# Kernel tuning notes

Measured on AMD Instinct MI355X. Metric: run time of the kernel, lower is better.

## Reference

```python
import jax, jax.numpy as jnp
import numpy as np
from jax import lax


def _causal_mask(shape, mask_center):
    # shape = (out_ch, in_ch, h, w); mirrors CausalConv2d mask construction
    o, i, h, w = shape
    m = np.zeros(shape, dtype=np.float32)
    m[:, :, : h // 2, :] = 1.0
    m[:, :, h // 2, : w // 2 + (0 if mask_center else 1)] = 1.0
    return jnp.asarray(m)

MASK1 = _causal_mask((16, 1, 7, 7), mask_center=True)
MASK2 = _causal_mask((16, 16, 3, 3), mask_center=False)


def _conv(x, w, b, pad):
    y = lax.conv_general_dilated(
        x, w, window_strides=(1, 1), padding=[(pad, pad), (pad, pad)],
        dimension_numbers=("NCHW", "OIHW", "NCHW"))
    return y + b[None, :, None, None]


def setup_inputs() -> dict:
    key = jax.random.key(0)
    ks = jax.random.split(key, 7)
    B, H, W = 1024, 64, 64
    x = jax.random.uniform(ks[0], (B, 1, H, W), dtype=jnp.float32)
    # Kaiming-ish init scales
    w1 = jax.random.normal(ks[1], (16, 1, 7, 7), jnp.float32) * (1.0 / np.sqrt(1 * 49))
    b1 = jax.random.normal(ks[2], (16,), jnp.float32) * 0.01
    w2 = jax.random.normal(ks[3], (16, 16, 3, 3), jnp.float32) * (1.0 / np.sqrt(16 * 9))
    b2 = jax.random.normal(ks[4], (16,), jnp.float32) * 0.01
    w3 = jax.random.normal(ks[5], (1, 16, 1, 1), jnp.float32) * (1.0 / np.sqrt(16))
    b3 = jax.random.normal(ks[6], (1,), jnp.float32) * 0.01
    return {"x": x, "w1": w1, "b1": b1, "w2": w2, "b2": b2, "w3": w3, "b3": b3}


def reference(x, w1, b1, w2, b2, w3, b3):
    # PixelCNN._forward: masked conv7x7 -> relu -> masked conv3x3 -> relu -> conv1x1 -> sigmoid
    h = jax.nn.relu(_conv(x, w1 * MASK1, b1, pad=3))
    h = jax.nn.relu(_conv(h, w2 * MASK2, b2, pad=1))
    return jax.nn.sigmoid(_conv(h, w3, b3, pad=0))
```

## Files before the change

kernel.cpp:

```cpp
#include <hip/hip_runtime.h>

typedef _Float16 half8  __attribute__((ext_vector_type(8)));
typedef __fp16   fp16x2 __attribute__((ext_vector_type(2)));
typedef float    floatx4 __attribute__((ext_vector_type(4)));

#define IMG_H 64
#define IMG_W 64
#define TH 16
#define TW 32
#define INW 40
#define H1W 34
#define NPX 640
#define CP 912
#define CPM1 911

__device__ __forceinline__ unsigned pk2u(float a, float b) {
    fp16x2 h = __builtin_amdgcn_cvt_pkrtz(a, b);
    return __builtin_bit_cast(unsigned, h);
}

__global__ __launch_bounds__(256, 8) void pixelcnn_mfma10(
    const float* __restrict__ x,
    const float* __restrict__ w1, const float* __restrict__ b1,
    const float* __restrict__ w2, const float* __restrict__ b2,
    const float* __restrict__ w3, const float* __restrict__ b3,
    float* __restrict__ out)
{
    __shared__ __align__(16) _Float16      s16[4 * CP];
    __shared__ __align__(16) _Float16      s_w1t[16 * 32];
    __shared__ __align__(16) unsigned char s_w2t8[16 * 96];
    __shared__ __align__(16) float         s_b1[16], s_b2[16], s_w3[16];
    __shared__ float                       s_b3;
    __shared__ __align__(16) unsigned      s_h1[2 * NPX * 2];

    const int t    = threadIdx.x;
    const int lane = t & 63;
    const int wave = t >> 6;
    const int n    = lane & 15;
    const int quad = lane >> 4;
    const int img  = blockIdx.y;
    const int btile = blockIdx.x;
    const int ty0 = (btile >> 1) * TH;
    const int tx0 = (btile & 1) * TW;

    const float* xim = x + img * (IMG_H * IMG_W);

    if (t < 210) {
        int r = t / 10, c4 = (t - r * 10) * 4;
        int gy = ty0 - 4 + r;
        int gx0 = tx0 - 4 + c4;
        float4 v  = {0.f, 0.f, 0.f, 0.f};
        float4 v2 = {0.f, 0.f, 0.f, 0.f};
        if ((unsigned)gy < IMG_H) {
            const float* rp = xim + gy * IMG_W;
            if ((unsigned)gx0 < IMG_W)       v  = *(const float4*)(rp + gx0);
            if ((unsigned)(gx0 + 4) < IMG_W) v2 = *(const float4*)(rp + gx0 + 4);
        }
        unsigned a0 = pk2u(v.x,  v.y),  a1 = pk2u(v.z,  v.w);
        unsigned a2 = pk2u(v2.x, v2.y), a3 = pk2u(v2.z, v2.w);
        unsigned m10 = (a0 >> 16) | (a1 << 16);
        unsigned m21 = (a1 >> 16) | (a2 << 16);
        unsigned m32 = (a2 >> 16) | (a3 << 16);
        int lin = r * INW + c4;
        *(uint2*)&s16[0*CP + 4 + lin + 0] = uint2{a0,  a1 };
        *(uint2*)&s16[1*CP + 3 + lin + 1] = uint2{m10, m21};
        *(uint2*)&s16[2*CP + 2 + lin + 2] = uint2{a1,  a2 };
        *(uint2*)&s16[3*CP + 1 + lin + 3] = uint2{m21, m32};
    }
    if (t < 192) {
        int c = t / 48, e = t - c * 48;
        s16[c * CP + (4 - c) + 840 + e] = (_Float16)0.f;
    }
    {
        int ch = t >> 4, l = t & 15;
        const float* w1c = w1 + ch * 49;
#pragma unroll
        for (int j2 = 0; j2 < 2; ++j2) {
            int k = l + 16 * j2, q = k >> 3, jj = k & 7;
            float v = 0.f;
            if (q < 3)      { if (jj < 7) v = w1c[q * 7 + jj]; }
            else            { if (jj < 3) v = w1c[21 + jj];    }
            s_w1t[ch * 32 + k] = (_Float16)v;
        }
        const float* w2cl = w2 + (ch * 16 + l) * 9;
#pragma unroll
        for (int j = 0; j < 6; ++j) {
            float v = (j < 5) ? w2cl[j] : 0.f;
            unsigned q8 = (unsigned)__builtin_amdgcn_cvt_pk_fp8_f32(v, 0.f, 0, false);
            s_w2t8[ch * 96 + j * 16 + l] = (unsigned char)(q8 & 0xff);
        }
    }
    if (t < 16) { s_b1[t] = b1[t]; s_b2[t] = b2[t]; s_w3[t] = w3[t]; }
    if (t == 16) s_b3 = b3[0];
    __syncthreads();

    {
        const half8 afrag = *(const half8*)&s_w1t[n * 32 + quad * 8];
        const floatx4 bias1 = ((const floatx4*)s_b1)[quad];
        int p  = wave * 16 + n;
        int py = (p >= H1W) ? 1 : 0;
        int px = p - py * H1W;
        int lin1p = (py + quad) * INW + px + 4;
        unsigned wd = (unsigned)((quad >> 1) * (NPX * 2) + p * 2 + (quad & 1));

#pragma unroll
        for (int i = 0; i < 10; ++i) {
            int c = px & 3;
            const _Float16* ap = &s16[c * CPM1 + lin1p];
            uint2 lo = *(const uint2*)ap;
            uint2 hi = *(const uint2*)(ap + 4);
            uint4 bu; bu.x = lo.x; bu.y = lo.y; bu.z = hi.x; bu.w = hi.y;
            half8 b = __builtin_bit_cast(half8, bu);
            floatx4 acc = bias1;
            acc = __builtin_amdgcn_mfma_f32_16x16x32_f16(afrag, b, acc, 0, 0, 0);
            int d = __builtin_amdgcn_cvt_pk_fp8_f32(fmaxf(acc[0], 0.f), fmaxf(acc[1], 0.f), 0, false);
            d = __builtin_amdgcn_cvt_pk_fp8_f32(fmaxf(acc[2], 0.f), fmaxf(acc[3], 0.f), d, true);
            s_h1[wd] = (unsigned)d;
            int px2 = px + 30;
            bool wrap = px2 >= H1W;
            px     = wrap ? px2 - H1W : px2;
            lin1p += wrap ? 76 : 70;
            wd    += 128;
        }
    }
    __syncthreads();

    {
        int cell = -1;
        if (t < 34)      { if (ty0 == 0) cell = t; }
        else if (t < 52) { cell = (t - 34) * H1W + ((tx0 == 0) ? 0 : 33); }
        if (cell >= 0) {
            *(uint2*)&s_h1[cell * 2]           = uint2{0u, 0u};
            *(uint2*)&s_h1[NPX * 2 + cell * 2] = uint2{0u, 0u};
        }
    }
    __syncthreads();

    {
        const long w2f0 = *(const long*)&s_w2t8[n * 96 +  0 + quad * 8];
        const long w2f1 = *(const long*)&s_w2t8[n * 96 + 32 + quad * 8];
        const long w2f2 = *(const long*)&s_w2t8[n * 96 + 64 + quad * 8];
        const floatx4 bias2 = ((const floatx4*)s_b2)[quad];
        const floatx4 w3q   = ((const floatx4*)s_w3)[quad];
        const float bias3 = s_b3;
        const int y0 = wave >> 1, x0 = (wave & 1) * 16;
        const int tqh = quad >> 1, plane = quad & 1;
        const int E0 = (y0 + 1) * H1W + x0 + n + 1;
        const char* h1b = (const char*)s_h1 + plane * (NPX * 8);
        const char* a0 = h1b + (E0 - 35 + tqh) * 8;
        const char* a1 = h1b + (E0 + (tqh ? -1 : -33)) * 8;
        const char* a2 = h1b + E0 * 8;
        float* sbase = out + ((img * IMG_H) + ty0 + y0 + 2 * quad) * IMG_W + tx0 + x0 + n;

#pragma unroll
        for (int g = 0; g < 2; ++g) {
            float sv0, sv1, sv2, sv3;
#pragma unroll
            for (int q = 0; q < 4; ++q) {
                const int k = g * 4 + q;
                floatx4 acc = bias2;
                acc = __builtin_amdgcn_mfma_f32_16x16x32_fp8_fp8(w2f0, *(const long*)(a0 + k * 544), acc, 0, 0, 0);
                acc = __builtin_amdgcn_mfma_f32_16x16x32_fp8_fp8(w2f1, *(const long*)(a1 + k * 544), acc, 0, 0, 0);
                acc = __builtin_amdgcn_mfma_f32_16x16x32_fp8_fp8(w2f2, *(const long*)(a2 + k * 544), acc, 0, 0, 0);
                float s = fmaxf(acc[0], 0.f) * w3q[0];
                s = fmaf(fmaxf(acc[1], 0.f), w3q[1], s);
                s = fmaf(fmaxf(acc[2], 0.f), w3q[2], s);
                s = fmaf(fmaxf(acc[3], 0.f), w3q[3], s);
                s += __shfl_xor(s, 16);
                s += __shfl_xor(s, 32);
                if      (q == 0) sv0 = s;
                else if (q == 1) sv1 = s;
                else if (q == 2) sv2 = s;
                else             sv3 = s;
            }
            float t01 = (quad & 1) ? sv1 : sv0;
            float t23 = (quad & 1) ? sv3 : sv2;
            float v   = (quad & 2) ? t23 : t01;
            float r = __builtin_amdgcn_rcpf(1.f + __expf(-(v + bias3)));
            *(float*)((char*)sbase + g * 2048) = r;
        }
    }
}

extern "C" void kernel_launch(void* const* d_in, const int* in_sizes, int n_in,
                              void* d_out, int out_size, void* d_ws, size_t ws_size,
                              hipStream_t stream) {
    const float* x  = (const float*)d_in[0];
    const float* w1 = (const float*)d_in[1];
    const float* b1 = (const float*)d_in[2];
    const float* w2 = (const float*)d_in[3];
    const float* b2 = (const float*)d_in[4];
    const float* w3 = (const float*)d_in[5];
    const float* b3 = (const float*)d_in[6];
    float* out = (float*)d_out;

    dim3 grid(8, 1024);
    dim3 block(256);
    hipLaunchKernelGGL(pixelcnn_mfma10, grid, block, 0, stream,
                       x, w1, b1, w2, b2, w3, b3, out);
}
```

Before: 108.5 us.

## Retile to full-width 8-row strips, removing column halos and a barrier

Each block now covers an 8x64 strip of the image instead of a 16x32 tile, so no left or right column halo is needed. The conv1 stage processes 9 rows of 66 columns with simpler, fixed addressing and no per-iteration wrap logic. Zeroing of the padding borders moves into the load phase and is handled by predication in the conv1 store, which removes one __syncthreads. The cost is a larger top/bottom halo relative to tile size, about 9/8 conv1 recompute instead of 10/8, with different LDS layout strides.

```diff
diff --git a/kernel.cpp b/kernel.cpp
--- a/kernel.cpp
+++ b/kernel.cpp
@@ -6,11 +6,12 @@
 
 #define IMG_H 64
 #define IMG_W 64
-#define TH 16
-#define TW 32
-#define INW 40
-#define H1W 34
-#define NPX 640
+#define TH 8
+#define INW 72
+#define INH 12
+#define H1W 66
+#define H1H 9
+#define PLDW (H1H*H1W*2)
 #define CP 912
 #define CPM1 911
 
@@ -19,7 +20,7 @@
     return __builtin_bit_cast(unsigned, h);
 }
 
-__global__ __launch_bounds__(256, 8) void pixelcnn_mfma10(
+__global__ __launch_bounds__(256, 8) void pixelcnn_mfma11(
     const float* __restrict__ x,
     const float* __restrict__ w1, const float* __restrict__ b1,
     const float* __restrict__ w2, const float* __restrict__ b2,
@@ -31,7 +32,7 @@
     __shared__ __align__(16) unsigned char s_w2t8[16 * 96];
     __shared__ __align__(16) float         s_b1[16], s_b2[16], s_w3[16];
     __shared__ float                       s_b3;
-    __shared__ __align__(16) unsigned      s_h1[2 * NPX * 2];
+    __shared__ __align__(16) unsigned      s_h1[2 * PLDW];
 
     const int t    = threadIdx.x;
     const int lane = t & 63;
@@ -39,16 +40,14 @@
     const int n    = lane & 15;
     const int quad = lane >> 4;
     const int img  = blockIdx.y;
-    const int btile = blockIdx.x;
-    const int ty0 = (btile >> 1) * TH;
-    const int tx0 = (btile & 1) * TW;
+    const int ty0  = blockIdx.x * TH;
 
     const float* xim = x + img * (IMG_H * IMG_W);
 
-    if (t < 210) {
-        int r = t / 10, c4 = (t - r * 10) * 4;
+    if (t < 216) {
+        int r = t / 18, c4 = (t - r * 18) * 4;
         int gy = ty0 - 4 + r;
-        int gx0 = tx0 - 4 + c4;
+        int gx0 = c4 - 4;
         float4 v  = {0.f, 0.f, 0.f, 0.f};
         float4 v2 = {0.f, 0.f, 0.f, 0.f};
         if ((unsigned)gy < IMG_H) {
@@ -62,14 +61,15 @@
         unsigned m21 = (a1 >> 16) | (a2 << 16);
         unsigned m32 = (a2 >> 16) | (a3 << 16);
         int lin = r * INW + c4;
-        *(uint2*)&s16[0*CP + 4 + lin + 0] = uint2{a0,  a1 };
-        *(uint2*)&s16[1*CP + 3 + lin + 1] = uint2{m10, m21};
-        *(uint2*)&s16[2*CP + 2 + lin + 2] = uint2{a1,  a2 };
-        *(uint2*)&s16[3*CP + 1 + lin + 3] = uint2{m21, m32};
-    }
-    if (t < 192) {
-        int c = t / 48, e = t - c * 48;
-        s16[c * CP + (4 - c) + 840 + e] = (_Float16)0.f;
+        *(uint2*)&s16[0*CP + 4 + lin] = uint2{a0,  a1 };
+        *(uint2*)&s16[1*CP + 4 + lin] = uint2{m10, m21};
+        *(uint2*)&s16[2*CP + 4 + lin] = uint2{a1,  a2 };
+        *(uint2*)&s16[3*CP + 4 + lin] = uint2{m21, m32};
+    } else if (t < 234) {
+        int idx = t - 216;
+        int cell = (idx >> 1) * H1W + ((idx & 1) ? 65 : 0);
+        *(uint2*)&s_h1[cell * 2]        = uint2{0u, 0u};
+        *(uint2*)&s_h1[PLDW + cell * 2] = uint2{0u, 0u};
     }
     {
         int ch = t >> 4, l = t & 15;
@@ -97,16 +97,16 @@
     {
         const half8 afrag = *(const half8*)&s_w1t[n * 32 + quad * 8];
         const floatx4 bias1 = ((const floatx4*)s_b1)[quad];
-        int p  = wave * 16 + n;
-        int py = (p >= H1W) ? 1 : 0;
-        int px = p - py * H1W;
-        int lin1p = (py + quad) * INW + px + 4;
-        unsigned wd = (unsigned)((quad >> 1) * (NPX * 2) + p * 2 + (quad & 1));
+        const int px = wave * 16 + n;
+        const int S  = px + 1;
+        const int c  = S & 3;
+        const _Float16* ap0 = &s16[c * CPM1 + 4 + S + quad * INW];
+        const unsigned wd0 = (unsigned)((quad >> 1) * PLDW + S * 2 + (quad & 1));
+        const bool top = (ty0 == 0);
 
 #pragma unroll
-        for (int i = 0; i < 10; ++i) {
-            int c = px & 3;
-            const _Float16* ap = &s16[c * CPM1 + lin1p];
+        for (int i = 0; i < H1H; ++i) {
+            const _Float16* ap = ap0 + i * INW;
             uint2 lo = *(const uint2*)ap;
             uint2 hi = *(const uint2*)(ap + 4);
             uint4 bu; bu.x = lo.x; bu.y = lo.y; bu.z = hi.x; bu.w = hi.y;
@@ -115,23 +115,9 @@
             acc = __builtin_amdgcn_mfma_f32_16x16x32_f16(afrag, b, acc, 0, 0, 0);
             int d = __builtin_amdgcn_cvt_pk_fp8_f32(fmaxf(acc[0], 0.f), fmaxf(acc[1], 0.f), 0, false);
             d = __builtin_amdgcn_cvt_pk_fp8_f32(fmaxf(acc[2], 0.f), fmaxf(acc[3], 0.f), d, true);
-            s_h1[wd] = (unsigned)d;
-            int px2 = px + 30;
-            bool wrap = px2 >= H1W;
-            px     = wrap ? px2 - H1W : px2;
-            lin1p += wrap ? 76 : 70;
-            wd    += 128;
-        }
-    }
-    __syncthreads();
-
-    {
-        int cell = -1;
-        if (t < 34)      { if (ty0 == 0) cell = t; }
-        else if (t < 52) { cell = (t - 34) * H1W + ((tx0 == 0) ? 0 : 33); }
-        if (cell >= 0) {
-            *(uint2*)&s_h1[cell * 2]           = uint2{0u, 0u};
-            *(uint2*)&s_h1[NPX * 2 + cell * 2] = uint2{0u, 0u};
+            unsigned dv = (unsigned)d;
+            if (i == 0) dv = top ? 0u : dv;
+            s_h1[wd0 + i * (H1W * 2)] = dv;
         }
     }
     __syncthreads();
@@ -143,14 +129,14 @@
         const floatx4 bias2 = ((const floatx4*)s_b2)[quad];
         const floatx4 w3q   = ((const floatx4*)s_w3)[quad];
         const float bias3 = s_b3;
-        const int y0 = wave >> 1, x0 = (wave & 1) * 16;
+        const int x0 = wave * 16;
         const int tqh = quad >> 1, plane = quad & 1;
-        const int E0 = (y0 + 1) * H1W + x0 + n + 1;
-        const char* h1b = (const char*)s_h1 + plane * (NPX * 8);
-        const char* a0 = h1b + (E0 - 35 + tqh) * 8;
-        const char* a1 = h1b + (E0 + (tqh ? -1 : -33)) * 8;
+        const int E0 = H1W + x0 + n + 1;
+        const char* h1b = (const char*)s_h1 + plane * (PLDW * 4);
+        const char* a0 = h1b + (E0 - H1W - 1 + tqh) * 8;
+        const char* a1 = h1b + (E0 + (tqh ? -1 : -(H1W - 1))) * 8;
         const char* a2 = h1b + E0 * 8;
-        float* sbase = out + ((img * IMG_H) + ty0 + y0 + 2 * quad) * IMG_W + tx0 + x0 + n;
+        float* sbase = out + ((img * IMG_H) + ty0 + quad) * IMG_W + x0 + n;
 
 #pragma unroll
         for (int g = 0; g < 2; ++g) {
@@ -159,9 +145,9 @@
             for (int q = 0; q < 4; ++q) {
                 const int k = g * 4 + q;
                 floatx4 acc = bias2;
-                acc = __builtin_amdgcn_mfma_f32_16x16x32_fp8_fp8(w2f0, *(const long*)(a0 + k * 544), acc, 0, 0, 0);
-                acc = __builtin_amdgcn_mfma_f32_16x16x32_fp8_fp8(w2f1, *(const long*)(a1 + k * 544), acc, 0, 0, 0);
-                acc = __builtin_amdgcn_mfma_f32_16x16x32_fp8_fp8(w2f2, *(const long*)(a2 + k * 544), acc, 0, 0, 0);
+                acc = __builtin_amdgcn_mfma_f32_16x16x32_fp8_fp8(w2f0, *(const long*)(a0 + k * 528), acc, 0, 0, 0);
+                acc = __builtin_amdgcn_mfma_f32_16x16x32_fp8_fp8(w2f1, *(const long*)(a1 + k * 528), acc, 0, 0, 0);
+                acc = __builtin_amdgcn_mfma_f32_16x16x32_fp8_fp8(w2f2, *(const long*)(a2 + k * 528), acc, 0, 0, 0);
                 float s = fmaxf(acc[0], 0.f) * w3q[0];
                 s = fmaf(fmaxf(acc[1], 0.f), w3q[1], s);
                 s = fmaf(fmaxf(acc[2], 0.f), w3q[2], s);
@@ -177,7 +163,7 @@
             float t23 = (quad & 1) ? sv3 : sv2;
             float v   = (quad & 2) ? t23 : t01;
             float r = __builtin_amdgcn_rcpf(1.f + __expf(-(v + bias3)));
-            *(float*)((char*)sbase + g * 2048) = r;
+            *(float*)((char*)sbase + g * 1024) = r;
         }
     }
 }
@@ -196,6 +182,6 @@
 
     dim3 grid(8, 1024);
     dim3 block(256);
-    hipLaunchKernelGGL(pixelcnn_mfma10, grid, block, 0, stream,
+    hipLaunchKernelGGL(pixelcnn_mfma11, grid, block, 0, stream,
                        x, w1, b1, w2, b2, w3, b3, out);
 }
```

Measured after the change: 105.1 us. 1.03x faster.
